# Optimization experiments

Hardware: AMD Instinct MI355X
Metric: run time of the kernel (lower is better)

The kernel has to match this reference:

```python
import jax, jax.numpy as jnp
import numpy as np

N_NODES = 50000
N_EDGES = 800000
N_GRAPHS = 100
IN_DIM = 100
OUT_DIM = 128
N_ETYPES = 4
N_STEPS = 8


def setup_inputs() -> dict:
    key = jax.random.key(0)
    ks = jax.random.split(key, 16)
    s = 0.05
    return {
        "features": jax.random.normal(ks[0], (N_NODES, IN_DIM), jnp.float32),
        "edge_src": jax.random.randint(ks[1], (N_EDGES,), 0, N_NODES, jnp.int32),
        "edge_dst": jax.random.randint(ks[2], (N_EDGES,), 0, N_NODES, jnp.int32),
        "edge_types": jax.random.randint(ks[3], (N_EDGES,), 0, N_ETYPES, jnp.int32),
        "graph_ids": jnp.sort(jax.random.randint(ks[4], (N_NODES,), 0, N_GRAPHS, jnp.int32)),
        "W_msg": jax.random.normal(ks[5], (N_ETYPES, OUT_DIM, OUT_DIM), jnp.float32) * s,
        "b_msg": jax.random.normal(ks[6], (N_ETYPES, OUT_DIM), jnp.float32) * s,
        "W_ih": jax.random.normal(ks[7], (3 * OUT_DIM, OUT_DIM), jnp.float32) * s,
        "W_hh": jax.random.normal(ks[8], (3 * OUT_DIM, OUT_DIM), jnp.float32) * s,
        "b_ih": jax.random.normal(ks[9], (3 * OUT_DIM,), jnp.float32) * s,
        "b_hh": jax.random.normal(ks[10], (3 * OUT_DIM,), jnp.float32) * s,
        "W1": jax.random.normal(ks[11], (256, OUT_DIM), jnp.float32) * s,
        "b1": jax.random.normal(ks[12], (256,), jnp.float32) * s,
        "W2": jax.random.normal(ks[13], (1, 256), jnp.float32) * s,
        "b2": jax.random.normal(ks[14], (1,), jnp.float32) * s,
    }


def _gru_cell(x, h, W_ih, W_hh, b_ih, b_hh):
    # torch.nn.GRUCell: gate order (reset, update, new)
    gi = x @ W_ih.T + b_ih  # [N, 3D]
    gh = h @ W_hh.T + b_hh
    i_r, i_z, i_n = jnp.split(gi, 3, axis=-1)
    h_r, h_z, h_n = jnp.split(gh, 3, axis=-1)
    r = jax.nn.sigmoid(i_r + h_r)
    z = jax.nn.sigmoid(i_z + h_z)
    n = jnp.tanh(i_n + r * h_n)
    return (1.0 - z) * n + z * h


def reference(features, edge_src, edge_dst, edge_types, graph_ids,
              W_msg, b_msg, W_ih, W_hh, b_ih, b_hh, W1, b1, W2, b2):
    n_nodes = features.shape[0]
    # DGL GatedGraphConv: zero-pad input features to out_feats
    h = jnp.pad(features, ((0, 0), (0, OUT_DIM - features.shape[1])))
    for _ in range(N_STEPS):
        # per-edge-type linear transform of source features: [T, N, D]
        transformed = jnp.einsum('nd,tdf->tnf', h, W_msg) + b_msg[:, None, :]
        msgs = transformed[edge_types, edge_src]  # [E, D] gather
        a = jax.ops.segment_sum(msgs, edge_dst, num_segments=n_nodes)  # scatter-add
        h = _gru_cell(a, h, W_ih, W_hh, b_ih, b_hh)
    # masked mean pooling per graph (mask_mean over de-batchified graphs)
    counts = jax.ops.segment_sum(jnp.ones((n_nodes,), h.dtype), graph_ids,
                                 num_segments=N_GRAPHS)
    sums = jax.ops.segment_sum(h, graph_ids, num_segments=N_GRAPHS)
    pooled = sums / jnp.maximum(counts, 1.0)[:, None]  # [B, D]
    # classifier: Linear -> relu -> (dropout: eval noop) -> Linear -> sigmoid
    hidden = jax.nn.relu(pooled @ W1.T + b1)
    logits = hidden @ W2.T + b2  # [B, 1]
    return jax.nn.sigmoid(logits).squeeze(-1)  # [B]
```

## Files before the change

kernel.cpp:

```cpp
#include <hip/hip_runtime.h>
#include <hip/hip_bf16.h>
#include <math.h>

#define N_NODES 50000
#define M_PAD   50048
#define N_EDGES 800000
#define N_GRAPHS 100
#define IN_DIM 100
#define D 128
#define N_STEPS 8
#define NBINS (N_NODES * 4)
#define SCAN_BLOCKS 196

typedef unsigned short ushort_t;
typedef __bf16 bf16x8 __attribute__((ext_vector_type(8)));
typedef float f32x4 __attribute__((ext_vector_type(4)));

__device__ inline ushort_t f2b(float f) {
  __hip_bfloat16 b = __float2bfloat16(f);
  return *reinterpret_cast<ushort_t*>(&b);
}
__device__ inline float b2f(unsigned int u16) {
  unsigned int x = u16 << 16;
  return __builtin_bit_cast(float, x);
}

__global__ void pad_kernel(const float* __restrict__ feat, float* __restrict__ h) {
  int idx = blockIdx.x * blockDim.x + threadIdx.x;
  if (idx >= N_NODES * D) return;
  int n = idx >> 7, d = idx & 127;
  h[idx] = (d < IN_DIM) ? feat[n * IN_DIM + d] : 0.0f;
}

__global__ void cast_h_kernel(const float* __restrict__ h, ushort_t* __restrict__ ah) {
  int idx = blockIdx.x * blockDim.x + threadIdx.x;
  if (idx >= N_NODES * D) return;
  int n = idx >> 7, d = idx & 127;
  ah[(size_t)n * 256 + 128 + d] = f2b(h[idx]);
}

__global__ void prep_bts(const float* __restrict__ W_msg, ushort_t* __restrict__ BtS) {
  int idx = blockIdx.x * blockDim.x + threadIdx.x;
  if (idx >= 128 * 512) return;
  int f = idx >> 9, kp = idx & 511;
  int t = kp >> 7, k = kp & 127;
  BtS[(size_t)f * 512 + kp] = f2b(W_msg[((size_t)t * 128 + k) * 128 + f]);
}

__global__ void prep_wg(const float* __restrict__ W_ih, const float* __restrict__ W_hh,
                        const float* __restrict__ b_ih, const float* __restrict__ b_hh,
                        ushort_t* __restrict__ WgT, float* __restrict__ gbias) {
  int idx = blockIdx.x * blockDim.x + threadIdx.x;
  if (idx >= 512 * 256) return;
  int colp = idx >> 8, k = idx & 255;
  int g = colp >> 6, gate = (colp >> 4) & 3, r = colp & 15;
  int d = g * 16 + r;
  float v;
  if (gate == 3)      v = (k < 128) ? 0.f : W_hh[(size_t)(256 + d) * 128 + (k - 128)];
  else if (gate == 2) v = (k < 128) ? W_ih[(size_t)(256 + d) * 128 + k] : 0.f;
  else {
    int j0 = (gate == 0) ? d : 128 + d;
    v = (k < 128) ? W_ih[(size_t)j0 * 128 + k] : W_hh[(size_t)j0 * 128 + (k - 128)];
  }
  WgT[(size_t)colp * 256 + k] = f2b(v);
  if (k == 0) {
    float bb = (gate == 0) ? b_ih[d] + b_hh[d]
             : (gate == 1) ? b_ih[128 + d] + b_hh[128 + d]
             : (gate == 2) ? b_ih[256 + d] : b_hh[256 + d];
    gbias[colp] = bb;
  }
}

__global__ void hist_kernel(const int* __restrict__ edst, const int* __restrict__ etype,
                            int* __restrict__ cnt2) {
  int e = blockIdx.x * 256 + threadIdx.x;
  if (e >= N_EDGES) return;
  atomicAdd(&cnt2[edst[e] * 4 + etype[e]], 1);
}

__global__ __launch_bounds__(1024) void scanA(const int* __restrict__ cnt2,
                                              int* __restrict__ tmp, int* __restrict__ bsum) {
  __shared__ int wsum[16];
  int b = blockIdx.x, t = threadIdx.x;
  int i = b * 1024 + t;
  int lane = t & 63, wid = t >> 6;
  int x = (i < NBINS) ? cnt2[i] : 0;
  #pragma unroll
  for (int s = 1; s < 64; s <<= 1) {
    int y = __shfl_up(x, s, 64);
    if (lane >= s) x += y;
  }
  if (lane == 63) wsum[wid] = x;
  __syncthreads();
  if (wid == 0) {
    int w = (lane < 16) ? wsum[lane] : 0;
    #pragma unroll
    for (int s = 1; s < 16; s <<= 1) {
      int y = __shfl_up(w, s, 64);
      if (lane >= s) w += y;
    }
    if (lane < 16) wsum[lane] = w;
  }
  __syncthreads();
  int wb = (wid > 0) ? wsum[wid - 1] : 0;
  tmp[i] = wb + x;
  if (t == 1023) bsum[b] = wsum[15];
}

__global__ __launch_bounds__(64) void scanB(const int* __restrict__ bsum,
                                            int* __restrict__ bpre) {
  int lane = threadIdx.x;
  int carry = 0;
  for (int base = 0; base < SCAN_BLOCKS; base += 64) {
    int idx = base + lane;
    int v = (idx < SCAN_BLOCKS) ? bsum[idx] : 0;
    int x = v;
    #pragma unroll
    for (int s = 1; s < 64; s <<= 1) {
      int y = __shfl_up(x, s, 64);
      if (lane >= s) x += y;
    }
    if (idx < SCAN_BLOCKS) bpre[idx] = carry + x - v;
    carry += __shfl(x, 63, 64);
  }
}

__global__ __launch_bounds__(1024) void scanC(const int* __restrict__ tmp,
                                              const int* __restrict__ bpre,
                                              int* __restrict__ offs2) {
  int b = blockIdx.x, t = threadIdx.x;
  int i = b * 1024 + t;
  if (i < NBINS) offs2[i + 1] = tmp[i] + bpre[b];
  if (i == 0) offs2[0] = 0;
}

__global__ void fill_kernel(const int* __restrict__ esrc, const int* __restrict__ edst,
                            const int* __restrict__ etype, const int* __restrict__ offs2,
                            int* __restrict__ cursor, int* __restrict__ payload) {
  int e = blockIdx.x * 256 + threadIdx.x;
  if (e >= N_EDGES) return;
  int key = edst[e] * 4 + etype[e];
  int pos = atomicAdd(&cursor[key], 1);
  payload[offs2[key] + pos] = esrc[e];
}

__global__ __launch_bounds__(256) void gather_kernel(const int* __restrict__ offs2,
    const int* __restrict__ payload, const ushort_t* __restrict__ hb,
    ushort_t* __restrict__ S, float* __restrict__ cntf) {
  int n = blockIdx.x * 4 + (threadIdx.x >> 6);
  int lane = threadIdx.x & 63;
  if (n >= N_NODES) return;
  int bb[5];
  #pragma unroll
  for (int k = 0; k < 5; ++k) bb[k] = offs2[n * 4 + k];
  float a[4][2] = {{0.f, 0.f}, {0.f, 0.f}, {0.f, 0.f}, {0.f, 0.f}};
  const ushort_t* hrow = hb + 128 + lane * 2;
  for (int base = bb[0]; base < bb[4]; base += 64) {
    int lim = min(bb[4], base + 64);
    int cnt = lim - base;
    int pe = (lane < cnt) ? payload[base + lane] : 0;
    #pragma unroll
    for (int t = 0; t < 4; ++t) {
      int lo = max(bb[t], base), hi = min(bb[t + 1], lim);
      int i = lo;
      for (; i + 4 <= hi; i += 4) {
        int s0 = __shfl(pe, i - base, 64);
        int s1 = __shfl(pe, i + 1 - base, 64);
        int s2 = __shfl(pe, i + 2 - base, 64);
        int s3 = __shfl(pe, i + 3 - base, 64);
        unsigned int u0 = *(const unsigned int*)(hrow + (size_t)s0 * 256);
        unsigned int u1 = *(const unsigned int*)(hrow + (size_t)s1 * 256);
        unsigned int u2 = *(const unsigned int*)(hrow + (size_t)s2 * 256);
        unsigned int u3 = *(const unsigned int*)(hrow + (size_t)s3 * 256);
        a[t][0] += b2f(u0 & 0xffff) + b2f(u1 & 0xffff) + b2f(u2 & 0xffff) + b2f(u3 & 0xffff);
        a[t][1] += b2f(u0 >> 16) + b2f(u1 >> 16) + b2f(u2 >> 16) + b2f(u3 >> 16);
      }
      for (; i < hi; ++i) {
        int s0 = __shfl(pe, i - base, 64);
        unsigned int u0 = *(const unsigned int*)(hrow + (size_t)s0 * 256);
        a[t][0] += b2f(u0 & 0xffff);
        a[t][1] += b2f(u0 >> 16);
      }
    }
  }
  #pragma unroll
  for (int t = 0; t < 4; ++t) {
    unsigned int packed = (unsigned int)f2b(a[t][0]) | ((unsigned int)f2b(a[t][1]) << 16);
    *(unsigned int*)(S + (size_t)n * 512 + t * 128 + lane * 2) = packed;
    if (lane == 0) cntf[n * 4 + t] = (float)(bb[t + 1] - bb[t]);
  }
}

template <int MODE>
__global__ __launch_bounds__(256) void mfma_gemm(
    const ushort_t* __restrict__ A, int lda, int K,
    const ushort_t* __restrict__ Bt,
    const float* __restrict__ bias, const float* __restrict__ b_msg,
    const float* __restrict__ cntf,
    ushort_t* __restrict__ ah_out, float* __restrict__ h) {
  __shared__ ushort_t As[128][40];
  __shared__ ushort_t Bs[128][40];
  const int m0 = blockIdx.x * 128, n0 = blockIdx.y * 128;
  int tid = threadIdx.x;
  int wave = tid >> 6, lane = tid & 63;
  int wm = (wave & 1) * 64, wn = (wave >> 1) * 64;
  int quad = lane >> 4, l16 = lane & 15;
  f32x4 acc[4][4];
  #pragma unroll
  for (int i = 0; i < 4; ++i)
    #pragma unroll
    for (int j = 0; j < 4; ++j) acc[i][j] = (f32x4){0.f, 0.f, 0.f, 0.f};

  for (int k0 = 0; k0 < K; k0 += 32) {
    #pragma unroll
    for (int i = 0; i < 2; ++i) {
      int r = (tid >> 2) + i * 64;
      int kc = (tid & 3) * 8;
      uint4 va = *(const uint4*)(A + (size_t)(m0 + r) * lda + k0 + kc);
      *(uint4*)&As[r][kc] = va;
      uint4 vb = *(const uint4*)(Bt + (size_t)(n0 + r) * K + k0 + kc);
      *(uint4*)&Bs[r][kc] = vb;
    }
    __syncthreads();
    bf16x8 af[4], bfr[4];
    #pragma unroll
    for (int i = 0; i < 4; ++i) af[i] = *(const bf16x8*)&As[wm + i * 16 + l16][quad * 8];
    #pragma unroll
    for (int j = 0; j < 4; ++j) bfr[j] = *(const bf16x8*)&Bs[wn + j * 16 + l16][quad * 8];
    #pragma unroll
    for (int i = 0; i < 4; ++i)
      #pragma unroll
      for (int j = 0; j < 4; ++j)
        acc[i][j] = __builtin_amdgcn_mfma_f32_16x16x32_bf16(af[i], bfr[j], acc[i][j], 0, 0, 0);
    __syncthreads();
  }

  if (MODE == 2) {
    float bm[4][4];
    #pragma unroll
    for (int j = 0; j < 4; ++j)
      #pragma unroll
      for (int t = 0; t < 4; ++t)
        bm[j][t] = b_msg[t * 128 + wn + j * 16 + l16];
    #pragma unroll
    for (int i = 0; i < 4; ++i)
      #pragma unroll
      for (int reg = 0; reg < 4; ++reg) {
        int m = m0 + wm + i * 16 + quad * 4 + reg;
        float4 c = *(const float4*)(cntf + (size_t)m * 4);
        #pragma unroll
        for (int j = 0; j < 4; ++j) {
          int n = wn + j * 16 + l16;
          float val = acc[i][j][reg] + c.x * bm[j][0] + c.y * bm[j][1]
                                     + c.z * bm[j][2] + c.w * bm[j][3];
          ah_out[(size_t)m * 256 + n] = f2b(val);
        }
      }
  } else {
    int dim = ((n0 + wn) >> 6) * 16 + l16;
    float br = bias[n0 + wn + l16];
    float bz = bias[n0 + wn + 16 + l16];
    float bi = bias[n0 + wn + 32 + l16];
    float bh = bias[n0 + wn + 48 + l16];
    #pragma unroll
    for (int i = 0; i < 4; ++i)
      #pragma unroll
      for (int reg = 0; reg < 4; ++reg) {
        int m = m0 + wm + i * 16 + quad * 4 + reg;
        float pr  = acc[i][0][reg] + br;
        float pz  = acc[i][1][reg] + bz;
        float in_ = acc[i][2][reg] + bi;
        float hn  = acc[i][3][reg] + bh;
        float r = 1.0f / (1.0f + expf(-pr));
        float z = 1.0f / (1.0f + expf(-pz));
        float nn = tanhf(in_ + r * hn);
        size_t hi = (size_t)m * 128 + dim;
        float hv = (1.0f - z) * nn + z * h[hi];
        h[hi] = hv;
        ah_out[(size_t)m * 256 + 128 + dim] = f2b(hv);
      }
  }
}

__global__ __launch_bounds__(128) void pool_kernel(const float* __restrict__ h,
    const int* __restrict__ gids, float* __restrict__ pooled, float* __restrict__ gcnt) {
  __shared__ int lo_s, hi_s;
  int g = blockIdx.x, c = blockIdx.y, d = threadIdx.x;
  if (d == 0) {
    int lo = 0, hi = N_NODES;
    while (lo < hi) { int mid = (lo + hi) >> 1; if (gids[mid] < g) lo = mid + 1; else hi = mid; }
    lo_s = lo;
    int lo2 = lo, hi2 = N_NODES;
    while (lo2 < hi2) { int mid = (lo2 + hi2) >> 1; if (gids[mid] < g + 1) lo2 = mid + 1; else hi2 = mid; }
    hi_s = lo2;
  }
  __syncthreads();
  int lo = lo_s, hi = hi_s;
  int len = hi - lo;
  int b = lo + (int)(((long long)len * c) >> 3);
  int e = lo + (int)(((long long)len * (c + 1)) >> 3);
  float s = 0.f;
  for (int n = b; n < e; ++n) s += h[(size_t)n * 128 + d];
  if (e > b) atomicAdd(&pooled[g * 128 + d], s);
  if (c == 0 && d == 0) gcnt[g] = (float)len;
}

__global__ __launch_bounds__(256) void classifier_kernel(
    const float* __restrict__ pooled, const float* __restrict__ gcnt,
    const float* __restrict__ W1, const float* __restrict__ b1,
    const float* __restrict__ W2, const float* __restrict__ b2,
    float* __restrict__ out) {
  __shared__ float p[D];
  __shared__ float hid[256];
  __shared__ float wsum[4];
  int g = blockIdx.x;
  int t = threadIdx.x;
  float cnt = fmaxf(gcnt[g], 1.0f);
  if (t < D) p[t] = pooled[g * D + t] / cnt;
  __syncthreads();
  float acc = b1[t];
  const float* w = W1 + (size_t)t * D;
  for (int k = 0; k < D; ++k) acc += p[k] * w[k];
  hid[t] = fmaxf(acc, 0.0f);
  __syncthreads();
  float v = hid[t] * W2[t];
  for (int off = 32; off > 0; off >>= 1) v += __shfl_down(v, off, 64);
  if ((t & 63) == 0) wsum[t >> 6] = v;
  __syncthreads();
  if (t == 0) {
    float s = wsum[0] + wsum[1] + wsum[2] + wsum[3] + b2[0];
    out[g] = 1.0f / (1.0f + expf(-s));
  }
}

extern "C" void kernel_launch(void* const* d_in, const int* in_sizes, int n_in,
                              void* d_out, int out_size, void* d_ws, size_t ws_size,
                              hipStream_t stream) {
  const float* features = (const float*)d_in[0];
  const int* esrc  = (const int*)d_in[1];
  const int* edst  = (const int*)d_in[2];
  const int* etype = (const int*)d_in[3];
  const int* gids  = (const int*)d_in[4];
  const float* W_msg = (const float*)d_in[5];
  const float* b_msg = (const float*)d_in[6];
  const float* W_ih  = (const float*)d_in[7];
  const float* W_hh  = (const float*)d_in[8];
  const float* b_ih  = (const float*)d_in[9];
  const float* b_hh  = (const float*)d_in[10];
  const float* W1 = (const float*)d_in[11];
  const float* b1 = (const float*)d_in[12];
  const float* W2 = (const float*)d_in[13];
  const float* b2 = (const float*)d_in[14];
  float* out = (float*)d_out;

  char* ws = (char*)d_ws;
  size_t off_b = 0;
  auto alloc = [&](size_t bytes) -> void* {
    void* p = ws + off_b;
    off_b += (bytes + 255) & ~(size_t)255;
    return p;
  };
  float*    h      = (float*)alloc((size_t)M_PAD * 128 * 4);
  ushort_t* ahA    = (ushort_t*)alloc((size_t)M_PAD * 256 * 2);
  ushort_t* ahB    = (ushort_t*)alloc((size_t)M_PAD * 256 * 2);
  ushort_t* S      = (ushort_t*)alloc((size_t)M_PAD * 512 * 2);
  float*    cntf   = (float*)alloc((size_t)M_PAD * 4 * 4);
  ushort_t* BtS    = (ushort_t*)alloc(128 * 512 * 2);
  ushort_t* WgT    = (ushort_t*)alloc(512 * 256 * 2);
  float*    gbias  = (float*)alloc(512 * 4);
  int*      cnt2   = (int*)alloc((size_t)NBINS * 4);
  int*      offs2  = (int*)alloc((size_t)(NBINS + 1) * 4);
  int*      cursor = (int*)alloc((size_t)NBINS * 4);
  int*      tmp    = (int*)alloc((size_t)SCAN_BLOCKS * 1024 * 4);
  int*      bsum   = (int*)alloc(SCAN_BLOCKS * 4);
  int*      bpre   = (int*)alloc(SCAN_BLOCKS * 4);
  int*      payload= (int*)alloc((size_t)N_EDGES * 4);
  float*    pooled = (float*)alloc(N_GRAPHS * 128 * 4);
  float*    gcnt   = (float*)alloc(N_GRAPHS * 4);

  pad_kernel<<<(N_NODES * 128 + 255) / 256, 256, 0, stream>>>(features, h);
  cast_h_kernel<<<(N_NODES * 128 + 255) / 256, 256, 0, stream>>>(h, ahA);
  prep_bts<<<(128 * 512 + 255) / 256, 256, 0, stream>>>(W_msg, BtS);
  prep_wg<<<(512 * 256 + 255) / 256, 256, 0, stream>>>(W_ih, W_hh, b_ih, b_hh, WgT, gbias);
  hipMemsetAsync(cnt2, 0, (size_t)NBINS * 4, stream);
  hipMemsetAsync(cursor, 0, (size_t)NBINS * 4, stream);
  hist_kernel<<<(N_EDGES + 255) / 256, 256, 0, stream>>>(edst, etype, cnt2);
  scanA<<<SCAN_BLOCKS, 1024, 0, stream>>>(cnt2, tmp, bsum);
  scanB<<<1, 64, 0, stream>>>(bsum, bpre);
  scanC<<<SCAN_BLOCKS, 1024, 0, stream>>>(tmp, bpre, offs2);
  fill_kernel<<<(N_EDGES + 255) / 256, 256, 0, stream>>>(esrc, edst, etype, offs2, cursor, payload);

  ushort_t* cur = ahA;
  ushort_t* nxt = ahB;
  for (int step = 0; step < N_STEPS; ++step) {
    gather_kernel<<<(N_NODES + 3) / 4, 256, 0, stream>>>(offs2, payload, cur, S, cntf);
    mfma_gemm<2><<<dim3(M_PAD / 128, 1), 256, 0, stream>>>(
        S, 512, 512, BtS, nullptr, b_msg, cntf, cur, nullptr);
    mfma_gemm<1><<<dim3(M_PAD / 128, 4), 256, 0, stream>>>(
        cur, 256, 256, WgT, gbias, nullptr, nullptr, nxt, h);
    ushort_t* t2 = cur; cur = nxt; nxt = t2;
  }

  hipMemsetAsync(pooled, 0, (size_t)N_GRAPHS * 128 * 4, stream);
  pool_kernel<<<dim3(N_GRAPHS, 8), 128, 0, stream>>>(h, gids, pooled, gcnt);
  classifier_kernel<<<N_GRAPHS, 256, 0, stream>>>(pooled, gcnt, W1, b1, W2, b2, out);
}
```

Before: 1.060 ms.

## Record atomic rank in histogram to drop fill atomics; flatten gather loop

The histogram kernel now stores each edge's atomicAdd return value as its rank, so the fill kernel writes payload positions directly without a second atomic pass or a cursor memset. The gather kernel replaces the per-edge-type inner loops with one flat 8-way unrolled loop over all of a node's edges, choosing the type accumulator by comparing against the bin boundaries. This aims to issue more independent loads per iteration and avoid short per-type loops. The cost is an extra rank array, plus select and branch logic on every edge.

```diff
diff --git a/kernel.cpp b/kernel.cpp
--- a/kernel.cpp
+++ b/kernel.cpp
@@ -72,10 +72,10 @@
 }
 
 __global__ void hist_kernel(const int* __restrict__ edst, const int* __restrict__ etype,
-                            int* __restrict__ cnt2) {
+                            int* __restrict__ cnt2, int* __restrict__ rank) {
   int e = blockIdx.x * 256 + threadIdx.x;
   if (e >= N_EDGES) return;
-  atomicAdd(&cnt2[edst[e] * 4 + etype[e]], 1);
+  rank[e] = atomicAdd(&cnt2[edst[e] * 4 + etype[e]], 1);
 }
 
 __global__ __launch_bounds__(1024) void scanA(const int* __restrict__ cnt2,
@@ -136,12 +136,11 @@
 
 __global__ void fill_kernel(const int* __restrict__ esrc, const int* __restrict__ edst,
                             const int* __restrict__ etype, const int* __restrict__ offs2,
-                            int* __restrict__ cursor, int* __restrict__ payload) {
+                            const int* __restrict__ rank, int* __restrict__ payload) {
   int e = blockIdx.x * 256 + threadIdx.x;
   if (e >= N_EDGES) return;
   int key = edst[e] * 4 + etype[e];
-  int pos = atomicAdd(&cursor[key], 1);
-  payload[offs2[key] + pos] = esrc[e];
+  payload[offs2[key] + rank[e]] = esrc[e];
 }
 
 __global__ __launch_bounds__(256) void gather_kernel(const int* __restrict__ offs2,
@@ -159,27 +158,37 @@
     int lim = min(bb[4], base + 64);
     int cnt = lim - base;
     int pe = (lane < cnt) ? payload[base + lane] : 0;
-    #pragma unroll
-    for (int t = 0; t < 4; ++t) {
-      int lo = max(bb[t], base), hi = min(bb[t + 1], lim);
-      int i = lo;
-      for (; i + 4 <= hi; i += 4) {
-        int s0 = __shfl(pe, i - base, 64);
-        int s1 = __shfl(pe, i + 1 - base, 64);
-        int s2 = __shfl(pe, i + 2 - base, 64);
-        int s3 = __shfl(pe, i + 3 - base, 64);
-        unsigned int u0 = *(const unsigned int*)(hrow + (size_t)s0 * 256);
-        unsigned int u1 = *(const unsigned int*)(hrow + (size_t)s1 * 256);
-        unsigned int u2 = *(const unsigned int*)(hrow + (size_t)s2 * 256);
-        unsigned int u3 = *(const unsigned int*)(hrow + (size_t)s3 * 256);
-        a[t][0] += b2f(u0 & 0xffff) + b2f(u1 & 0xffff) + b2f(u2 & 0xffff) + b2f(u3 & 0xffff);
-        a[t][1] += b2f(u0 >> 16) + b2f(u1 >> 16) + b2f(u2 >> 16) + b2f(u3 >> 16);
+    int i = base;
+    for (; i + 8 <= lim; i += 8) {
+      unsigned int u[8];
+      #pragma unroll
+      for (int q = 0; q < 8; ++q) {
+        int s = __shfl(pe, i + q - base, 64);
+        u[q] = *(const unsigned int*)(hrow + (size_t)s * 256);
       }
-      for (; i < hi; ++i) {
-        int s0 = __shfl(pe, i - base, 64);
-        unsigned int u0 = *(const unsigned int*)(hrow + (size_t)s0 * 256);
-        a[t][0] += b2f(u0 & 0xffff);
-        a[t][1] += b2f(u0 >> 16);
+      #pragma unroll
+      for (int q = 0; q < 8; ++q) {
+        int ii = i + q;
+        int ti = (ii >= bb[1]) + (ii >= bb[2]) + (ii >= bb[3]);
+        float v0 = b2f(u[q] & 0xffff), v1 = b2f(u[q] >> 16);
+        switch (ti) {
+          case 0: a[0][0] += v0; a[0][1] += v1; break;
+          case 1: a[1][0] += v0; a[1][1] += v1; break;
+          case 2: a[2][0] += v0; a[2][1] += v1; break;
+          default: a[3][0] += v0; a[3][1] += v1; break;
+        }
+      }
+    }
+    for (; i < lim; ++i) {
+      int s = __shfl(pe, i - base, 64);
+      unsigned int u0 = *(const unsigned int*)(hrow + (size_t)s * 256);
+      int ti = (i >= bb[1]) + (i >= bb[2]) + (i >= bb[3]);
+      float v0 = b2f(u0 & 0xffff), v1 = b2f(u0 >> 16);
+      switch (ti) {
+        case 0: a[0][0] += v0; a[0][1] += v1; break;
+        case 1: a[1][0] += v0; a[1][1] += v1; break;
+        case 2: a[2][0] += v0; a[2][1] += v1; break;
+        default: a[3][0] += v0; a[3][1] += v1; break;
       }
     }
   }
@@ -370,7 +379,7 @@
   float*    gbias  = (float*)alloc(512 * 4);
   int*      cnt2   = (int*)alloc((size_t)NBINS * 4);
   int*      offs2  = (int*)alloc((size_t)(NBINS + 1) * 4);
-  int*      cursor = (int*)alloc((size_t)NBINS * 4);
+  int*      rank   = (int*)alloc((size_t)N_EDGES * 4);
   int*      tmp    = (int*)alloc((size_t)SCAN_BLOCKS * 1024 * 4);
   int*      bsum   = (int*)alloc(SCAN_BLOCKS * 4);
   int*      bpre   = (int*)alloc(SCAN_BLOCKS * 4);
@@ -383,12 +392,11 @@
   prep_bts<<<(128 * 512 + 255) / 256, 256, 0, stream>>>(W_msg, BtS);
   prep_wg<<<(512 * 256 + 255) / 256, 256, 0, stream>>>(W_ih, W_hh, b_ih, b_hh, WgT, gbias);
   hipMemsetAsync(cnt2, 0, (size_t)NBINS * 4, stream);
-  hipMemsetAsync(cursor, 0, (size_t)NBINS * 4, stream);
-  hist_kernel<<<(N_EDGES + 255) / 256, 256, 0, stream>>>(edst, etype, cnt2);
+  hist_kernel<<<(N_EDGES + 255) / 256, 256, 0, stream>>>(edst, etype, cnt2, rank);
   scanA<<<SCAN_BLOCKS, 1024, 0, stream>>>(cnt2, tmp, bsum);
   scanB<<<1, 64, 0, stream>>>(bsum, bpre);
   scanC<<<SCAN_BLOCKS, 1024, 0, stream>>>(tmp, bpre, offs2);
-  fill_kernel<<<(N_EDGES + 255) / 256, 256, 0, stream>>>(esrc, edst, etype, offs2, cursor, payload);
+  fill_kernel<<<(N_EDGES + 255) / 256, 256, 0, stream>>>(esrc, edst, etype, offs2, rank, payload);
 
   ushort_t* cur = ahA;
   ushort_t* nxt = ahB;
```

Measured after the change: 1.469 ms. +38.5%, slower.
